# Kernel optimization log

Measured on AMD Instinct MI355X. Metric: run time of the kernel, lower is better.

Reference implementation:

```python
import jax, jax.numpy as jnp
import numpy as np

B, S, HID = 2, 2048, 2048
NH, NKV, HD = 16, 4, 128
G = NH // NKV  # kv group size
EPS = 1e-6


def setup_inputs() -> dict:
    key = jax.random.key(0)
    ks = jax.random.split(key, 7)
    w = 0.02
    return {
        "hidden_states": jax.random.normal(ks[0], (B, S, HID), dtype=jnp.float32),
        "position_ids": jnp.broadcast_to(jnp.arange(S, dtype=jnp.int64), (B, S)),
        "Wq": jax.random.normal(ks[1], (2 * NH * HD, HID), dtype=jnp.float32) * w,
        "Wk": jax.random.normal(ks[2], (NKV * HD, HID), dtype=jnp.float32) * w,
        "Wv": jax.random.normal(ks[3], (NKV * HD, HID), dtype=jnp.float32) * w,
        "Wo": jax.random.normal(ks[4], (HID, NH * HD), dtype=jnp.float32) * w,
        "norm_w": jnp.zeros((HID,), dtype=jnp.float32),
    }


def reference(hidden_states, position_ids, Wq, Wk, Wv, Wo, norm_w):
    # RMSNorm (weight parameterized as 1 + w, per source)
    ms = jnp.mean(hidden_states * hidden_states, axis=-1, keepdims=True)
    x = hidden_states * jax.lax.rsqrt(ms + EPS) * (1.0 + norm_w)

    qg = x @ Wq.T                                   # (B,S,2*NH*HD)
    q, gate = jnp.split(qg, 2, axis=-1)
    q = q.reshape(B, S, NH, HD).transpose(0, 2, 1, 3)       # (B,NH,S,HD)
    gate = gate.reshape(B, S, NH, HD).transpose(0, 2, 1, 3)
    k = (x @ Wk.T).reshape(B, S, NKV, HD).transpose(0, 2, 1, 3)  # (B,NKV,S,HD)
    v = (x @ Wv.T).reshape(B, S, NKV, HD).transpose(0, 2, 1, 3)

    scale = 1.0 / np.sqrt(HD).astype(np.float32)
    qg4 = q.reshape(B, NKV, G, S, HD)
    attn = jnp.einsum("bkgqd,bkld->bkgql", qg4, k) * scale   # (B,NKV,G,S,S)
    p = jax.nn.softmax(attn, axis=-1)
    o = jnp.einsum("bkgql,bkld->bkgqd", p, v).reshape(B, NH, S, HD)

    o = o * jax.nn.sigmoid(gate)                    # output gate
    o = o.transpose(0, 2, 1, 3).reshape(B, S, NH * HD)
    return o @ Wo.T
```

## Files before the change

kernel.cpp:

```cpp
#include <hip/hip_runtime.h>
#include <math.h>

#define BB    2
#define SS    2048
#define HIDD  2048
#define NHH   16
#define NKVV  4
#define HDD   128
#define MROWS 4096
#define QG_N  4096
#define KV_N  512
#define O_N   2048
#define KDIM  2048
#define EPS_  1e-6f
#define SCALE_ 0.08838834764831845f

typedef __attribute__((ext_vector_type(8))) __bf16 bf16x8;
typedef __attribute__((ext_vector_type(8))) unsigned short u16x8;
typedef __attribute__((ext_vector_type(4))) float f32x4;

__device__ __forceinline__ unsigned short f2bf(float f) {
  return __builtin_bit_cast(unsigned short, (__bf16)f);
}

__global__ __launch_bounds__(256) void f2bf_all(const float* __restrict__ Wq,
                                                const float* __restrict__ Wk,
                                                const float* __restrict__ Wv,
                                                const float* __restrict__ Wo,
                                                unsigned short* __restrict__ dst) {
  const int s0 = QG_N * KDIM / 4;
  const int s1 = s0 + KV_N * KDIM / 4;
  const int s2 = s1 + KV_N * KDIM / 4;
  const int s3 = s2 + O_N * KDIM / 4;
  int i = blockIdx.x * 256 + threadIdx.x;
  if (i >= s3) return;
  float4 v;
  if (i < s0)      v = ((const float4*)Wq)[i];
  else if (i < s1) v = ((const float4*)Wk)[i - s0];
  else if (i < s2) v = ((const float4*)Wv)[i - s1];
  else             v = ((const float4*)Wo)[i - s2];
  ushort4 u;
  u.x = f2bf(v.x); u.y = f2bf(v.y); u.z = f2bf(v.z); u.w = f2bf(v.w);
  ((ushort4*)dst)[i] = u;
}

__global__ __launch_bounds__(256) void rmsnorm_k(const float* __restrict__ h,
                                                 const float* __restrict__ w,
                                                 unsigned short* __restrict__ x) {
  int row = blockIdx.x;
  int t = threadIdx.x;
  const float4* hr = (const float4*)(h + (size_t)row * HIDD);
  const float4* w4 = (const float4*)w;

  float4 v0 = hr[t], v1 = hr[t + 256];
  float ss = v0.x*v0.x + v0.y*v0.y + v0.z*v0.z + v0.w*v0.w
           + v1.x*v1.x + v1.y*v1.y + v1.z*v1.z + v1.w*v1.w;
#pragma unroll
  for (int off = 32; off > 0; off >>= 1) ss += __shfl_down(ss, off, 64);

  __shared__ float part[4];
  __shared__ float rs_sh;
  if ((t & 63) == 0) part[t >> 6] = ss;
  __syncthreads();
  if (t == 0) rs_sh = rsqrtf((part[0]+part[1]+part[2]+part[3]) * (1.0f/HIDD) + EPS_);
  __syncthreads();
  float rs = rs_sh;

  float4 w0 = w4[t], w1 = w4[t + 256];
  ushort4 o0, o1;
  o0.x = f2bf(v0.x * rs * (1.f + w0.x));
  o0.y = f2bf(v0.y * rs * (1.f + w0.y));
  o0.z = f2bf(v0.z * rs * (1.f + w0.z));
  o0.w = f2bf(v0.w * rs * (1.f + w0.w));
  o1.x = f2bf(v1.x * rs * (1.f + w1.x));
  o1.y = f2bf(v1.y * rs * (1.f + w1.y));
  o1.z = f2bf(v1.z * rs * (1.f + w1.z));
  o1.w = f2bf(v1.w * rs * (1.f + w1.w));
  ushort4* xr = (ushort4*)(x + (size_t)row * HIDD);
  xr[t] = o0;
  xr[t + 256] = o1;
}

template <int OBF>
__device__ __forceinline__ void gemm_core(const unsigned short* __restrict__ Ab,
                                          const unsigned short* __restrict__ Bb,
                                          void* __restrict__ Cv,
                                          void* __restrict__ Cv2,
                                          int Ndim, int bm, int bn,
                                          unsigned short* Als, unsigned short* Bls) {
  char* ldsA = (char*)Als;
  char* ldsB = (char*)Bls;

  int t   = threadIdx.x;
  int r15 = t & 15;
  int g   = (t & 63) >> 4;
  int w   = t >> 6;
  int wr  = w >> 1, wc = w & 1;

  f32x4 acc[4][4] = {};

  for (int k0 = 0; k0 < KDIM; k0 += 64) {
    __syncthreads();
#pragma unroll
    for (int it = 0; it < 4; ++it) {
      int f      = it * 256 + t;
      int row    = f >> 3;
      int schunk = (f & 7) ^ (row & 7);
      unsigned ldsbase = (unsigned)((it * 256 + (w << 6)) << 4);
      __builtin_amdgcn_global_load_lds(
          (const unsigned int*)(Ab + ((size_t)(bm + row) << 11) + k0 + schunk * 8),
          (unsigned int*)(ldsA + ldsbase), 16, 0, 0);
      __builtin_amdgcn_global_load_lds(
          (const unsigned int*)(Bb + ((size_t)(bn + row) << 11) + k0 + schunk * 8),
          (unsigned int*)(ldsB + ldsbase), 16, 0, 0);
    }
    __syncthreads();

#pragma unroll
    for (int tt = 0; tt < 2; ++tt) {
      bf16x8 af[4], bfv[4];
#pragma unroll
      for (int mi = 0; mi < 4; ++mi) {
        int row = wr * 64 + mi * 16 + r15;
        af[mi] = *(const bf16x8*)(ldsA + row * 128 + (((4 * tt + g) ^ (row & 7)) << 4));
      }
#pragma unroll
      for (int ni = 0; ni < 4; ++ni) {
        int row = wc * 64 + ni * 16 + r15;
        bfv[ni] = *(const bf16x8*)(ldsB + row * 128 + (((4 * tt + g) ^ (row & 7)) << 4));
      }
      __builtin_amdgcn_s_setprio(1);
#pragma unroll
      for (int mi = 0; mi < 4; ++mi)
#pragma unroll
        for (int ni = 0; ni < 4; ++ni)
          acc[mi][ni] = __builtin_amdgcn_mfma_f32_16x16x32_bf16(af[mi], bfv[ni], acc[mi][ni], 0, 0, 0);
      __builtin_amdgcn_s_setprio(0);
    }
  }

#pragma unroll
  for (int mi = 0; mi < 4; ++mi)
#pragma unroll
    for (int ni = 0; ni < 4; ++ni) {
      int col = bn + wc * 64 + ni * 16 + r15;
#pragma unroll
      for (int r = 0; r < 4; ++r) {
        int rowg = bm + wr * 64 + mi * 16 + g * 4 + r;
        if (OBF == 1)
          ((unsigned short*)Cv)[(size_t)rowg * Ndim + col] = f2bf(acc[mi][ni][r]);
        else if (OBF == 2) {
          if (col < O_N)
            ((unsigned short*)Cv)[(size_t)rowg * O_N + col] = f2bf(acc[mi][ni][r] * SCALE_);
          else
            ((float*)Cv2)[(size_t)rowg * O_N + (col - O_N)] = acc[mi][ni][r];
        } else if (OBF == 3)
          ((unsigned short*)Cv)[(size_t)col * MROWS + rowg] = f2bf(acc[mi][ni][r]);
        else
          ((float*)Cv)[(size_t)rowg * Ndim + col] = acc[mi][ni][r];
      }
    }
}

template <int OBF>
__global__ __launch_bounds__(256) void gemm_bf16(const unsigned short* __restrict__ Ab,
                                                 const unsigned short* __restrict__ Bb,
                                                 void* __restrict__ Cv,
                                                 int Ndim) {
  __shared__ unsigned short Als[128 * 64];
  __shared__ unsigned short Bls[128 * 64];
  gemm_core<OBF>(Ab, Bb, Cv, nullptr, Ndim, blockIdx.y * 128, blockIdx.x * 128, Als, Bls);
}

__global__ __launch_bounds__(256) void gemm_qg(const unsigned short* __restrict__ Ab,
                                               const unsigned short* __restrict__ Bb,
                                               unsigned short* __restrict__ Cq,
                                               float* __restrict__ Cg) {
  __shared__ unsigned short Als[128 * 64];
  __shared__ unsigned short Bls[128 * 64];
  gemm_core<2>(Ab, Bb, (void*)Cq, (void*)Cg, QG_N, blockIdx.y * 128, blockIdx.x * 128, Als, Bls);
}

__global__ __launch_bounds__(256) void gemm_kv(const unsigned short* __restrict__ Ab,
                                               const unsigned short* __restrict__ Wk,
                                               const unsigned short* __restrict__ Wv,
                                               unsigned short* __restrict__ Ck,
                                               unsigned short* __restrict__ Cvt) {
  __shared__ unsigned short Als[128 * 64];
  __shared__ unsigned short Bls[128 * 64];
  int bx = blockIdx.x;
  if (bx < 4)
    gemm_core<1>(Ab, Wk, (void*)Ck, nullptr, KV_N, blockIdx.y * 128, bx * 128, Als, Bls);
  else
    gemm_core<3>(Ab, Wv, (void*)Cvt, nullptr, KV_N, blockIdx.y * 128, (bx & 3) * 128, Als, Bls);
}

__global__ __launch_bounds__(256, 2) void attn_mfma(const unsigned short* __restrict__ qb,
                                                    const float* __restrict__ gateb,
                                                    const unsigned short* __restrict__ kb,
                                                    const unsigned short* __restrict__ vt,
                                                    unsigned short* __restrict__ obuf) {
  __shared__ unsigned short Ks[2][64 * 128];
  __shared__ unsigned short Vt[2][128 * 64];
  char* ldsK0 = (char*)Ks;
  char* ldsV0 = (char*)Vt;

  int t = threadIdx.x;
  int l = t & 63, w = t >> 6;
  int c15 = l & 15, g = l >> 4;
  int bid = blockIdx.x;
  int swz = (bid & 7) * 64 + (bid >> 3);
  int qt = swz & 15, h = (swz >> 4) & 15, b = swz >> 8;
  int kh = h >> 2;
  size_t rowQ0 = (size_t)b * SS + (size_t)qt * 128;
  size_t rowKbase = (size_t)b * SS;

  bf16x8 qf[2][4];
#pragma unroll
  for (int qi = 0; qi < 2; ++qi)
#pragma unroll
    for (int ks = 0; ks < 4; ++ks)
      qf[qi][ks] = *(const bf16x8*)(qb + (rowQ0 + w * 32 + qi * 16 + c15) * O_N
                                       + h * HDD + g * 8 + ks * 32);

  f32x4 accO[2][8] = {};
  float mrun[2] = {-INFINITY, -INFINITY};
  float lrun[2] = {0.f, 0.f};

#define ISSUE_K(bufi, kt_)                                                     \
  {                                                                            \
    size_t rowK0 = rowKbase + (size_t)(kt_) * 64;                              \
    _Pragma("unroll")                                                          \
    for (int it = 0; it < 4; ++it) {                                           \
      int f = it * 256 + t;                                                    \
      int kv = f >> 4;                                                         \
      int schunk = (f & 15) ^ (kv & 7);                                        \
      unsigned ldsbase = (unsigned)((it * 256 + (w << 6)) << 4);               \
      __builtin_amdgcn_global_load_lds(                                        \
          (const unsigned int*)(kb + (rowK0 + kv) * KV_N + kh * HDD + schunk * 8), \
          (unsigned int*)(ldsK0 + (bufi) * 16384 + ldsbase), 16, 0, 0);        \
    }                                                                          \
  }
#define ISSUE_VT(bufi, kt_)                                                    \
  {                                                                            \
    size_t tokbase = rowKbase + (size_t)(kt_) * 64;                            \
    _Pragma("unroll")                                                          \
    for (int it = 0; it < 4; ++it) {                                           \
      int f = it * 256 + t;                                                    \
      int row = f >> 3;                                                        \
      int schunk = (f & 7) ^ (row & 7);                                        \
      unsigned ldsbase = (unsigned)((it * 256 + (w << 6)) << 4);               \
      __builtin_amdgcn_global_load_lds(                                        \
          (const unsigned int*)(vt + (size_t)(kh * 128 + row) * MROWS + tokbase + schunk * 8), \
          (unsigned int*)(ldsV0 + (bufi) * 16384 + ldsbase), 16, 0, 0);        \
    }                                                                          \
  }

  ISSUE_K(0, 0);
  ISSUE_VT(0, 0);
  asm volatile("s_waitcnt vmcnt(0)" ::: "memory");
  __syncthreads();

  const int NT = SS / 64;
  for (int kt = 0; kt < NT; ++kt) {
    int cur = kt & 1, nxt = cur ^ 1;
    char* ldsK = ldsK0 + cur * 16384;
    char* ldsV = ldsV0 + cur * 16384;

    if (kt + 1 < NT) {
      ISSUE_K(nxt, kt + 1);
      ISSUE_VT(nxt, kt + 1);
    }

    f32x4 accS[2][4] = {};
    __builtin_amdgcn_s_setprio(1);
#pragma unroll
    for (int nf = 0; nf < 4; ++nf) {
      int kvr = nf * 16 + c15;
#pragma unroll
      for (int ks = 0; ks < 4; ++ks) {
        bf16x8 kf = *(const bf16x8*)(ldsK + kvr * 256 + ((((g + 4 * ks) ^ (kvr & 7)) << 4)));
#pragma unroll
        for (int qi = 0; qi < 2; ++qi)
          accS[qi][nf] = __builtin_amdgcn_mfma_f32_16x16x32_bf16(kf, qf[qi][ks], accS[qi][nf], 0, 0, 0);
      }
    }
    __builtin_amdgcn_s_setprio(0);

    float mt[2];
#pragma unroll
    for (int qi = 0; qi < 2; ++qi) {
      float m0 = fmaxf(fmaxf(accS[qi][0][0], accS[qi][0][1]), fmaxf(accS[qi][0][2], accS[qi][0][3]));
#pragma unroll
      for (int nf = 1; nf < 4; ++nf)
        m0 = fmaxf(m0, fmaxf(fmaxf(accS[qi][nf][0], accS[qi][nf][1]), fmaxf(accS[qi][nf][2], accS[qi][nf][3])));
      m0 = fmaxf(m0, __shfl_xor(m0, 16, 64));
      m0 = fmaxf(m0, __shfl_xor(m0, 32, 64));
      mt[qi] = m0;
    }

    bool safe = (mt[0] <= mrun[0] + 8.f) && (mt[1] <= mrun[1] + 8.f);
    if (!__all(safe)) {
#pragma unroll
      for (int qi = 0; qi < 2; ++qi) {
        float mnew = fmaxf(mrun[qi], mt[qi]);
        float al = __expf(mrun[qi] - mnew);
        mrun[qi] = mnew;
        lrun[qi] *= al;
        float alr[4];
#pragma unroll
        for (int r = 0; r < 4; ++r) alr[r] = __shfl(al, g * 4 + r, 16);
#pragma unroll
        for (int df = 0; df < 8; ++df)
#pragma unroll
          for (int r = 0; r < 4; ++r) accO[qi][df][r] *= alr[r];
      }
    }

    u16x8 pfr[2][2];
#pragma unroll
    for (int qi = 0; qi < 2; ++qi) {
      float ps = 0.f;
#pragma unroll
      for (int nf = 0; nf < 4; ++nf) {
        float p0 = __expf(accS[qi][nf][0] - mrun[qi]);
        float p1 = __expf(accS[qi][nf][1] - mrun[qi]);
        float p2 = __expf(accS[qi][nf][2] - mrun[qi]);
        float p3 = __expf(accS[qi][nf][3] - mrun[qi]);
        ps += (p0 + p1) + (p2 + p3);
        pfr[qi][nf >> 1][(nf & 1) * 4 + 0] = f2bf(p0);
        pfr[qi][nf >> 1][(nf & 1) * 4 + 1] = f2bf(p1);
        pfr[qi][nf >> 1][(nf & 1) * 4 + 2] = f2bf(p2);
        pfr[qi][nf >> 1][(nf & 1) * 4 + 3] = f2bf(p3);
      }
      ps += __shfl_xor(ps, 16, 64);
      ps += __shfl_xor(ps, 32, 64);
      lrun[qi] += ps;
    }

    __builtin_amdgcn_s_setprio(1);
#pragma unroll
    for (int ks2 = 0; ks2 < 2; ++ks2) {
      bf16x8 pf0 = __builtin_bit_cast(bf16x8, pfr[0][ks2]);
      bf16x8 pf1 = __builtin_bit_cast(bf16x8, pfr[1][ks2]);
      int c0 = 4 * ks2 + (g >> 1);
      int half8 = (g & 1) * 8;
#pragma unroll
      for (int df = 0; df < 8; ++df) {
        int d = df * 16 + c15;
        const char* vrow = ldsV + d * 128;
        ushort4 lo = *(const ushort4*)(vrow + (((c0)     ^ (d & 7)) << 4) + half8);
        ushort4 hi = *(const ushort4*)(vrow + (((c0 + 2) ^ (d & 7)) << 4) + half8);
        u16x8 v8 = {lo.x, lo.y, lo.z, lo.w, hi.x, hi.y, hi.z, hi.w};
        bf16x8 vf = __builtin_bit_cast(bf16x8, v8);
        accO[0][df] = __builtin_amdgcn_mfma_f32_16x16x32_bf16(pf0, vf, accO[0][df], 0, 0, 0);
        accO[1][df] = __builtin_amdgcn_mfma_f32_16x16x32_bf16(pf1, vf, accO[1][df], 0, 0, 0);
      }
    }
    __builtin_amdgcn_s_setprio(0);

    if (kt + 1 < NT) {
      asm volatile("s_waitcnt vmcnt(0)" ::: "memory");
    }
    __syncthreads();
  }

#pragma unroll
  for (int qi = 0; qi < 2; ++qi) {
    float invL = 1.f / lrun[qi];
    float ivr[4];
#pragma unroll
    for (int r = 0; r < 4; ++r) ivr[r] = __shfl(invL, g * 4 + r, 16);
#pragma unroll
    for (int r = 0; r < 4; ++r) {
      size_t row = rowQ0 + w * 32 + qi * 16 + g * 4 + r;
#pragma unroll
      for (int df = 0; df < 8; ++df) {
        int d = df * 16 + c15;
        float gt = gateb[row * (size_t)O_N + h * HDD + d];
        float sg = 1.f / (1.f + __expf(-gt));
        obuf[row * (size_t)O_N + h * HDD + d] = f2bf(accO[qi][df][r] * ivr[r] * sg);
      }
    }
  }
#undef ISSUE_K
#undef ISSUE_VT
}

extern "C" void kernel_launch(void* const* d_in, const int* in_sizes, int n_in,
                              void* d_out, int out_size, void* d_ws, size_t ws_size,
                              hipStream_t stream) {
  const float* hs = (const float*)d_in[0];
  const float* Wq = (const float*)d_in[2];
  const float* Wk = (const float*)d_in[3];
  const float* Wv = (const float*)d_in[4];
  const float* Wo = (const float*)d_in[5];
  const float* nw = (const float*)d_in[6];
  float* out = (float*)d_out;

  float* gateb = (float*)d_ws;
  unsigned short* qb16 = (unsigned short*)(gateb + (size_t)MROWS * O_N);
  unsigned short* kb16 = qb16 + (size_t)MROWS * O_N;
  unsigned short* vt16 = kb16 + (size_t)MROWS * KV_N;
  unsigned short* xb   = vt16 + (size_t)KV_N * MROWS;
  unsigned short* ob   = xb   + (size_t)MROWS * HIDD;
  unsigned short* wqb  = ob   + (size_t)MROWS * O_N;
  unsigned short* wkb  = wqb  + (size_t)QG_N * KDIM;
  unsigned short* wvb  = wkb  + (size_t)KV_N * KDIM;
  unsigned short* wob  = wvb  + (size_t)KV_N * KDIM;

  const int tot4 = (QG_N + KV_N + KV_N + O_N) * KDIM / 4;
  f2bf_all<<<(tot4 + 255) / 256, 256, 0, stream>>>(Wq, Wk, Wv, Wo, wqb);
  rmsnorm_k<<<MROWS, 256, 0, stream>>>(hs, nw, xb);

  gemm_qg<<<dim3(QG_N/128, MROWS/128), 256, 0, stream>>>(xb, wqb, qb16, gateb);
  gemm_kv<<<dim3(8, MROWS/128), 256, 0, stream>>>(xb, wkb, wvb, kb16, vt16);
  attn_mfma<<<dim3(512), 256, 0, stream>>>(qb16, gateb, kb16, vt16, ob);
  gemm_bf16<0><<<dim3(O_N/128, MROWS/128), 256, 0, stream>>>(ob, wob, out, O_N);
}
```

Measured before the change: 283.9 us.

## Replace QG projection GEMM with 256x256-tile double-buffered direct-to-LDS kernel

The Q/gate projection GEMM moves from 128x128 tiles with 256 threads to a dedicated 256x256-tile kernel with 512 threads. It uses global_load_lds into double-buffered, XOR-swizzled LDS and interleaves staging of the next K tiles with MFMA quads under explicit vmcnt waits and barriers. The aim is more data reuse per loaded byte and overlap of global loads with matrix math in the largest GEMM. In exchange it uses 128KB of LDS per block and a fixed 64-step K schedule, and the grid drops to 256 blocks, which may underfill the device.

```diff
diff --git a/kernel.cpp b/kernel.cpp
--- a/kernel.cpp
+++ b/kernel.cpp
@@ -85,7 +85,6 @@
 __device__ __forceinline__ void gemm_core(const unsigned short* __restrict__ Ab,
                                           const unsigned short* __restrict__ Bb,
                                           void* __restrict__ Cv,
-                                          void* __restrict__ Cv2,
                                           int Ndim, int bm, int bn,
                                           unsigned short* Als, unsigned short* Bls) {
   char* ldsA = (char*)Als;
@@ -149,12 +148,7 @@
         int rowg = bm + wr * 64 + mi * 16 + g * 4 + r;
         if (OBF == 1)
           ((unsigned short*)Cv)[(size_t)rowg * Ndim + col] = f2bf(acc[mi][ni][r]);
-        else if (OBF == 2) {
-          if (col < O_N)
-            ((unsigned short*)Cv)[(size_t)rowg * O_N + col] = f2bf(acc[mi][ni][r] * SCALE_);
-          else
-            ((float*)Cv2)[(size_t)rowg * O_N + (col - O_N)] = acc[mi][ni][r];
-        } else if (OBF == 3)
+        else if (OBF == 3)
           ((unsigned short*)Cv)[(size_t)col * MROWS + rowg] = f2bf(acc[mi][ni][r]);
         else
           ((float*)Cv)[(size_t)rowg * Ndim + col] = acc[mi][ni][r];
@@ -169,16 +163,7 @@
                                                  int Ndim) {
   __shared__ unsigned short Als[128 * 64];
   __shared__ unsigned short Bls[128 * 64];
-  gemm_core<OBF>(Ab, Bb, Cv, nullptr, Ndim, blockIdx.y * 128, blockIdx.x * 128, Als, Bls);
-}
-
-__global__ __launch_bounds__(256) void gemm_qg(const unsigned short* __restrict__ Ab,
-                                               const unsigned short* __restrict__ Bb,
-                                               unsigned short* __restrict__ Cq,
-                                               float* __restrict__ Cg) {
-  __shared__ unsigned short Als[128 * 64];
-  __shared__ unsigned short Bls[128 * 64];
-  gemm_core<2>(Ab, Bb, (void*)Cq, (void*)Cg, QG_N, blockIdx.y * 128, blockIdx.x * 128, Als, Bls);
+  gemm_core<OBF>(Ab, Bb, Cv, Ndim, blockIdx.y * 128, blockIdx.x * 128, Als, Bls);
 }
 
 __global__ __launch_bounds__(256) void gemm_kv(const unsigned short* __restrict__ Ab,
@@ -190,9 +175,146 @@
   __shared__ unsigned short Bls[128 * 64];
   int bx = blockIdx.x;
   if (bx < 4)
-    gemm_core<1>(Ab, Wk, (void*)Ck, nullptr, KV_N, blockIdx.y * 128, bx * 128, Als, Bls);
+    gemm_core<1>(Ab, Wk, (void*)Ck, KV_N, blockIdx.y * 128, bx * 128, Als, Bls);
   else
-    gemm_core<3>(Ab, Wv, (void*)Cvt, nullptr, KV_N, blockIdx.y * 128, (bx & 3) * 128, Als, Bls);
+    gemm_core<3>(Ab, Wv, (void*)Cvt, KV_N, blockIdx.y * 128, (bx & 3) * 128, Als, Bls);
+}
+
+#define LD8(basep, r, x) \
+  (*(const bf16x8*)((basep) + (size_t)(r) * 128 + ((((x) ^ ((r)&7))) << 4)))
+
+#define STAGE_A(bufi, h, tk)                                                   \
+  { _Pragma("unroll")                                                          \
+    for (int c = 0; c < 2; ++c) {                                              \
+      int f = c * 512 + t;                                                     \
+      int rr = f >> 3;                                                         \
+      int sc = (f & 7) ^ (rr & 7);                                             \
+      __builtin_amdgcn_global_load_lds(                                        \
+        (const unsigned int*)(Ab + ((size_t)(bm + (h)*128 + rr) << 11) + (tk)*64 + sc*8), \
+        (unsigned int*)(lds8 + (bufi)*32768 + (h)*16384 + c*8192 + (w<<10)), 16, 0, 0); \
+    } }
+
+#define STAGE_B(bufi, h, tk)                                                   \
+  { _Pragma("unroll")                                                          \
+    for (int c = 0; c < 2; ++c) {                                              \
+      int f = c * 512 + t;                                                     \
+      int rr = f >> 3;                                                         \
+      int sc = (f & 7) ^ (rr & 7);                                             \
+      __builtin_amdgcn_global_load_lds(                                        \
+        (const unsigned int*)(Bbp + ((size_t)(bn + (h)*128 + rr) << 11) + (tk)*64 + sc*8), \
+        (unsigned int*)(lds8 + 65536 + (bufi)*32768 + (h)*16384 + c*8192 + (w<<10)), 16, 0, 0); \
+    } }
+
+#define RD_A(SRC, MIBASE)                                                      \
+  { _Pragma("unroll")                                                          \
+    for (int mi = 0; mi < 4; ++mi) {                                           \
+      int rr = wr * 128 + ((MIBASE) + mi) * 16 + r15;                          \
+      afr[mi][0] = LD8(SRC, rr, g);                                            \
+      afr[mi][1] = LD8(SRC, rr, 4 + g);                                        \
+    } }
+
+#define RD_B(SRC, NIBASE, DST)                                                 \
+  { _Pragma("unroll")                                                          \
+    for (int ni = 0; ni < 2; ++ni) {                                           \
+      int rr = wc * 64 + ((NIBASE) + ni) * 16 + r15;                           \
+      DST[ni][0] = LD8(SRC, rr, g);                                            \
+      DST[ni][1] = LD8(SRC, rr, 4 + g);                                        \
+    } }
+
+#define MFMA_QUAD(MIBASE, NIBASE, BREG)                                        \
+  { __builtin_amdgcn_s_setprio(1);                                             \
+    _Pragma("unroll")                                                          \
+    for (int mi = 0; mi < 4; ++mi)                                             \
+      _Pragma("unroll")                                                        \
+      for (int ni = 0; ni < 2; ++ni)                                           \
+        _Pragma("unroll")                                                      \
+        for (int ks = 0; ks < 2; ++ks)                                         \
+          acc[(MIBASE)+mi][(NIBASE)+ni] =                                      \
+            __builtin_amdgcn_mfma_f32_16x16x32_bf16(afr[mi][ks], BREG[ni][ks], \
+                                                    acc[(MIBASE)+mi][(NIBASE)+ni], 0, 0, 0); \
+    __builtin_amdgcn_s_setprio(0); }
+
+#define BAR() __builtin_amdgcn_s_barrier()
+
+__global__ __launch_bounds__(512, 2) void gemm_qg256(const unsigned short* __restrict__ Ab,
+                                                     const unsigned short* __restrict__ Bbp,
+                                                     unsigned short* __restrict__ Cq,
+                                                     float* __restrict__ Cg) {
+  __shared__ char lds8[131072];
+  int t = threadIdx.x;
+  int r15 = t & 15, g = (t & 63) >> 4, w = t >> 6;
+  int wr = w >> 2, wc = w & 3;
+  int bm = blockIdx.y * 256, bn = blockIdx.x * 256;
+  char* A0 = lds8;            char* A1 = lds8 + 32768;
+  char* B0 = lds8 + 65536;    char* B1 = lds8 + 98304;
+
+  f32x4 acc[8][4] = {};
+  bf16x8 afr[4][2], b0r[2][2], b1r[2][2];
+
+  STAGE_A(0, 0, 0); STAGE_A(0, 1, 0); STAGE_B(0, 0, 0); STAGE_B(0, 1, 0);
+  STAGE_A(1, 0, 1); STAGE_A(1, 1, 1); STAGE_B(1, 0, 1); STAGE_B(1, 1, 1);
+  asm volatile("s_waitcnt vmcnt(8)" ::: "memory");
+  BAR();
+
+  for (int i = 0; i < 15; ++i) {
+    int te = 2 * i + 2, to = 2 * i + 3;
+    RD_A(A0, 0); RD_B(B0, 0, b0r);
+    BAR(); MFMA_QUAD(0, 0, b0r); BAR();
+    RD_B(B0, 2, b1r);
+    BAR(); MFMA_QUAD(0, 2, b1r); BAR();
+    RD_A(A0, 4);
+    STAGE_B(0, 0, te);
+    BAR(); MFMA_QUAD(4, 0, b0r); BAR();
+    STAGE_A(0, 0, te);
+    BAR(); MFMA_QUAD(4, 2, b1r);
+    asm volatile("s_waitcnt vmcnt(4)" ::: "memory");
+    BAR();
+    RD_A(A1, 0); RD_B(B1, 0, b0r);
+    STAGE_A(0, 1, te);
+    BAR(); MFMA_QUAD(0, 0, b0r); BAR();
+    RD_B(B1, 2, b1r);
+    STAGE_B(0, 1, te);
+    BAR(); MFMA_QUAD(0, 2, b1r); BAR();
+    RD_A(A1, 4);
+    STAGE_B(1, 0, to); STAGE_B(1, 1, to);
+    BAR(); MFMA_QUAD(4, 0, b0r); BAR();
+    STAGE_A(1, 0, to); STAGE_A(1, 1, to);
+    BAR(); MFMA_QUAD(4, 2, b1r);
+    asm volatile("s_waitcnt vmcnt(8)" ::: "memory");
+    BAR();
+  }
+  RD_A(A0, 0); RD_B(B0, 0, b0r);
+  BAR(); MFMA_QUAD(0, 0, b0r); BAR();
+  RD_B(B0, 2, b1r);
+  BAR(); MFMA_QUAD(0, 2, b1r); BAR();
+  RD_A(A0, 4);
+  BAR(); MFMA_QUAD(4, 0, b0r); BAR();
+  BAR(); MFMA_QUAD(4, 2, b1r);
+  asm volatile("s_waitcnt vmcnt(0)" ::: "memory");
+  BAR();
+  RD_A(A1, 0); RD_B(B1, 0, b0r);
+  BAR(); MFMA_QUAD(0, 0, b0r); BAR();
+  RD_B(B1, 2, b1r);
+  BAR(); MFMA_QUAD(0, 2, b1r); BAR();
+  RD_A(A1, 4);
+  BAR(); MFMA_QUAD(4, 0, b0r); BAR();
+  BAR(); MFMA_QUAD(4, 2, b1r);
+
+  bool isq = (bn < O_N);
+  int colbase = bn + wc * 64;
+#pragma unroll
+  for (int mi = 0; mi < 8; ++mi) {
+    size_t row = (size_t)bm + wr * 128 + mi * 16 + g * 4;
+#pragma unroll
+    for (int ni = 0; ni < 4; ++ni) {
+      int col = colbase + ni * 16 + r15;
+#pragma unroll
+      for (int r = 0; r < 4; ++r) {
+        if (isq) Cq[(row + r) * O_N + col] = f2bf(acc[mi][ni][r] * SCALE_);
+        else     Cg[(row + r) * O_N + (col - O_N)] = acc[mi][ni][r];
+      }
+    }
+  }
 }
 
 __global__ __launch_bounds__(256, 2) void attn_mfma(const unsigned short* __restrict__ qb,
@@ -413,7 +535,7 @@
   f2bf_all<<<(tot4 + 255) / 256, 256, 0, stream>>>(Wq, Wk, Wv, Wo, wqb);
   rmsnorm_k<<<MROWS, 256, 0, stream>>>(hs, nw, xb);
 
-  gemm_qg<<<dim3(QG_N/128, MROWS/128), 256, 0, stream>>>(xb, wqb, qb16, gateb);
+  gemm_qg256<<<dim3(QG_N/256, MROWS/256), 512, 0, stream>>>(xb, wqb, qb16, gateb);
   gemm_kv<<<dim3(8, MROWS/128), 256, 0, stream>>>(xb, wkb, wvb, kb16, vt16);
   attn_mfma<<<dim3(512), 256, 0, stream>>>(qb16, gateb, kb16, vt16, ob);
   gemm_bf16<0><<<dim3(O_N/128, MROWS/128), 256, 0, stream>>>(ob, wob, out, O_N);
```

Measured after the change: 262.4 us. -7.6%, faster.
